# Kernel tuning notes

Hardware: AMD Instinct MI355X
Metric: run time of the kernel (lower is better)

Reference implementation:

```python
import jax, jax.numpy as jnp
import numpy as np

EMBED, HEADS, LEVELS, POINTS = 256, 8, 3, 4
HD = EMBED // HEADS
SHAPES = [(200, 200), (100, 100), (50, 50)]


def layer_norm(x, g, b, eps=1e-5):
    m = x.mean(-1, keepdims=True)
    v = ((x - m) ** 2).mean(-1, keepdims=True)
    return (x - m) * jax.lax.rsqrt(v + eps) * g + b


def bilinear_sample(v, loc, H, W):
    """v: (bs, H*W, heads, hd); loc: (bs, nq, heads, P, 2) normalized to [0,1].
    Matches F.grid_sample(bilinear, align_corners=False, padding_mode='zeros')
    applied to grid = 2*loc - 1. Returns (bs, nq, heads, P, hd)."""
    bs, nq, heads, P, _ = loc.shape
    hd = v.shape[-1]
    x = loc[..., 0] * W - 0.5
    y = loc[..., 1] * H - 0.5
    x0 = jnp.floor(x); y0 = jnp.floor(y)
    tx = x - x0; ty = y - y0
    x0i = x0.astype(jnp.int32); y0i = y0.astype(jnp.int32)
    vT = v.transpose(0, 2, 1, 3)  # (bs, heads, HW, hd)
    out = jnp.zeros((bs, heads, nq * P, hd), v.dtype)
    for dy, wy in ((0, 1.0 - ty), (1, ty)):
        for dx, wx in ((0, 1.0 - tx), (1, tx)):
            xi = x0i + dx; yi = y0i + dy
            valid = (xi >= 0) & (xi < W) & (yi >= 0) & (yi < H)
            idx = jnp.clip(yi, 0, H - 1) * W + jnp.clip(xi, 0, W - 1)
            w = (wx * wy * valid).transpose(0, 2, 1, 3).reshape(bs, heads, nq * P)
            idxT = idx.transpose(0, 2, 1, 3).reshape(bs, heads, nq * P)
            g = jnp.take_along_axis(vT, idxT[..., None], axis=2)  # (bs,heads,nqP,hd)
            out = out + w[..., None] * g
    return out.reshape(bs, heads, nq, P, hd).transpose(0, 2, 1, 3, 4)


def reference(query, value, query_pos, ref_pts, spatial_shapes, level_start_index,
              norm1_g, norm1_b, W_off, b_off, W_attn, b_attn, W_val, b_val,
              W_out, b_out, norm2_g, norm2_b, W1, b1, W2, b2):
    shapes = np.asarray(spatial_shapes)
    bs, nq, _ = query.shape
    # --- MultiScaleDeformableAttention on norm1(query) ---
    q = layer_norm(query, norm1_g, norm1_b)
    identity = q
    qp = q + query_pos
    offsets = (qp @ W_off + b_off).reshape(bs, nq, HEADS, LEVELS, POINTS, 2)
    aw = (qp @ W_attn + b_attn).reshape(bs, nq, HEADS, LEVELS * POINTS)
    aw = jax.nn.softmax(aw, axis=-1).reshape(bs, nq, HEADS, LEVELS, POINTS)
    v = (value @ W_val + b_val).reshape(bs, -1, HEADS, HD)
    # offset normalizer is (W, H) per level
    normalizer = jnp.stack([spatial_shapes[:, 1], spatial_shapes[:, 0]], -1).astype(query.dtype)
    loc = ref_pts[:, :, None, :, None, :] + offsets / normalizer[None, None, None, :, None, :]
    out = jnp.zeros((bs, nq, HEADS, HD), query.dtype)
    start = 0
    for l in range(LEVELS):
        H, W = int(shapes[l, 0]), int(shapes[l, 1])
        vl = v[:, start:start + H * W]
        s = bilinear_sample(vl, loc[:, :, :, l], H, W)  # (bs,nq,heads,P,hd)
        out = out + jnp.einsum('bqhpd,bqhp->bqhd', s, aw[:, :, :, l])
        start += H * W
    attn_out = out.reshape(bs, nq, EMBED) @ W_out + b_out + identity
    x = query + attn_out
    # --- FFN ---
    h = layer_norm(x, norm2_g, norm2_b)
    ffn = jax.nn.gelu(h @ W1 + b1, approximate=False) @ W2 + b2
    return x + ffn


def setup_inputs() -> dict:
    key = jax.random.key(0)
    ks = jax.random.split(key, 16)
    bs, nq = 1, 40000
    nv = sum(h * w for h, w in SHAPES)
    d = EMBED
    inp = {
        'query': jax.random.normal(ks[0], (bs, nq, d), jnp.float32),
        'value': jax.random.normal(ks[1], (bs, nv, d), jnp.float32),
        'query_pos': jax.random.normal(ks[2], (bs, nq, d), jnp.float32),
        'ref_pts': jax.random.uniform(ks[3], (bs, nq, LEVELS, 2), jnp.float32),
        'spatial_shapes': jnp.array(SHAPES, dtype=jnp.int32),
        'level_start_index': jnp.array(np.cumsum([0] + [h * w for h, w in SHAPES[:-1]]), dtype=jnp.int32),
    }
    s = 1.0 / np.sqrt(d)
    inp.update({
        'norm1_g': jnp.ones((d,), jnp.float32), 'norm1_b': jnp.zeros((d,), jnp.float32),
        'W_off': jax.random.normal(ks[4], (d, HEADS * LEVELS * POINTS * 2), jnp.float32) * 0.01,
        'b_off': jax.random.normal(ks[5], (HEADS * LEVELS * POINTS * 2,), jnp.float32) * 0.5,
        'W_attn': jax.random.normal(ks[6], (d, HEADS * LEVELS * POINTS), jnp.float32) * s,
        'b_attn': jnp.zeros((HEADS * LEVELS * POINTS,), jnp.float32),
        'W_val': jax.random.normal(ks[7], (d, d), jnp.float32) * s,
        'b_val': jnp.zeros((d,), jnp.float32),
        'W_out': jax.random.normal(ks[8], (d, d), jnp.float32) * s,
        'b_out': jnp.zeros((d,), jnp.float32),
        'norm2_g': jnp.ones((d,), jnp.float32), 'norm2_b': jnp.zeros((d,), jnp.float32),
        'W1': jax.random.normal(ks[9], (d, 4 * d), jnp.float32) * s,
        'b1': jnp.zeros((4 * d,), jnp.float32),
        'W2': jax.random.normal(ks[10], (4 * d, d), jnp.float32) / np.sqrt(4 * d),
        'b2': jnp.zeros((d,), jnp.float32),
    })
    return inp
```

## Files before the change

kernel.cpp:

```cpp
#include <hip/hip_runtime.h>
#include <hip/hip_bf16.h>
#include <math.h>

#define NQ 40000
#define NV 52500
#define D 256
#define NHEAD 8
#define HD 32
#define GUARD 512

using bf16x8 = __attribute__((ext_vector_type(8))) short;
using f32x4  = __attribute__((ext_vector_type(4))) float;
typedef int v2i32 __attribute__((ext_vector_type(2)));

__device__ __forceinline__ short f2bf(float f) {
  union { __hip_bfloat16 h; short s; } u;
  u.h = __float2bfloat16(f);
  return u.s;
}
__device__ __forceinline__ float bf2f(unsigned short s) {
  return __uint_as_float((unsigned)s << 16);
}
__device__ __forceinline__ unsigned pack2(float lo, float hi) {
  return (unsigned)(unsigned short)f2bf(lo) |
         ((unsigned)(unsigned short)f2bf(hi) << 16);
}
__device__ __forceinline__ void gload16(const void* g, void* l) {
  __builtin_amdgcn_global_load_lds(
      (const __attribute__((address_space(1))) unsigned int*)g,
      (__attribute__((address_space(3))) unsigned int*)l, 16, 0, 0);
}

template<int IMM>
__device__ __forceinline__ float swz_add(float x) {
  return x + __int_as_float(__builtin_amdgcn_ds_swizzle(__float_as_int(x), IMM));
}

__global__ __launch_bounds__(256) void k_prep(const float* __restrict__ Woff,
                                              const float* __restrict__ Wattn,
                                              const float* __restrict__ Wval,
                                              const float* __restrict__ Wout,
                                              const float* __restrict__ W1,
                                              const float* __restrict__ W2,
                                              const float* __restrict__ boff,
                                              const float* __restrict__ battn,
                                              short* __restrict__ WT288,
                                              short* __restrict__ WTval,
                                              short* __restrict__ WTout,
                                              short* __restrict__ WT1,
                                              short* __restrict__ WT2,
                                              float* __restrict__ bias288) {
  int idx = blockIdx.x * 256 + threadIdx.x;
  if (idx < 49152) {
    int n = idx >> 8, k = idx & 255;
    WT288[idx] = f2bf(Woff[k * 192 + n]);
  } else if (idx < 73728) {
    int li = idx - 49152; int n = li >> 8, k = li & 255;
    WT288[49152 + li] = f2bf(Wattn[k * 96 + n]);
  } else if (idx < 139264) {
    int li = idx - 73728; int n = li >> 8, k = li & 255;
    WTval[li] = f2bf(Wval[k * 256 + n]);
  } else if (idx < 204800) {
    int li = idx - 139264; int n = li >> 8, k = li & 255;
    WTout[li] = f2bf(Wout[k * 256 + n]);
  } else if (idx < 466944) {
    int li = idx - 204800; int n = li >> 8, k = li & 255;
    WT1[li] = f2bf(W1[k * 1024 + n]);
  } else if (idx < 729088) {
    int li = idx - 466944; int n = li >> 10, k = li & 1023;
    WT2[li] = f2bf(W2[k * 256 + n]);
  } else if (idx < 729376) {
    int i = idx - 729088;
    bias288[i] = (i < 192) ? boff[i] : battn[i - 192];
  }
}

__global__ __launch_bounds__(256) void k_ln1(const float* __restrict__ qin,
                                             const float* __restrict__ qpos,
                                             const float* __restrict__ g,
                                             const float* __restrict__ b,
                                             short* __restrict__ id_out,
                                             short* __restrict__ qp_out) {
  int wave = threadIdx.x >> 6;
  int lane = threadIdx.x & 63;
  int row  = blockIdx.x * 4 + wave;
  float4 x = ((const float4*)(qin + (size_t)row * D))[lane];
  float s  = x.x + x.y + x.z + x.w;
  float ss = x.x*x.x + x.y*x.y + x.z*x.z + x.w*x.w;
  for (int o = 32; o > 0; o >>= 1) { s += __shfl_down(s, o); ss += __shfl_down(ss, o); }
  s  = __shfl(s, 0);
  ss = __shfl(ss, 0);
  float m   = s * (1.0f / 256.0f);
  float var = ss * (1.0f / 256.0f) - m * m;
  float rs  = rsqrtf(var + 1e-5f);
  float4 gg = ((const float4*)g)[lane];
  float4 bb = ((const float4*)b)[lane];
  float4 qn;
  qn.x = (x.x - m) * rs * gg.x + bb.x;
  qn.y = (x.y - m) * rs * gg.y + bb.y;
  qn.z = (x.z - m) * rs * gg.z + bb.z;
  qn.w = (x.w - m) * rs * gg.w + bb.w;
  short4 io;
  io.x = f2bf(qn.x); io.y = f2bf(qn.y); io.z = f2bf(qn.z); io.w = f2bf(qn.w);
  ((short4*)(id_out + (size_t)row * D))[lane] = io;
  float4 p = ((const float4*)(qpos + (size_t)row * D))[lane];
  short4 o;
  o.x = f2bf(qn.x + p.x); o.y = f2bf(qn.y + p.y);
  o.z = f2bf(qn.z + p.z); o.w = f2bf(qn.w + p.w);
  ((short4*)(qp_out + (size_t)row * D))[lane] = o;
}

__global__ __launch_bounds__(256) void k_ln2(const float* __restrict__ xin,
                                             const float* __restrict__ g,
                                             const float* __restrict__ b,
                                             short* __restrict__ h_out) {
  int wave = threadIdx.x >> 6;
  int lane = threadIdx.x & 63;
  int row  = blockIdx.x * 4 + wave;
  float4 x = ((const float4*)(xin + (size_t)row * D))[lane];
  float s  = x.x + x.y + x.z + x.w;
  float ss = x.x*x.x + x.y*x.y + x.z*x.z + x.w*x.w;
  for (int o = 32; o > 0; o >>= 1) { s += __shfl_down(s, o); ss += __shfl_down(ss, o); }
  s  = __shfl(s, 0);
  ss = __shfl(ss, 0);
  float m   = s * (1.0f / 256.0f);
  float var = ss * (1.0f / 256.0f) - m * m;
  float rs  = rsqrtf(var + 1e-5f);
  float4 gg = ((const float4*)g)[lane];
  float4 bb = ((const float4*)b)[lane];
  short4 o;
  o.x = f2bf((x.x - m) * rs * gg.x + bb.x);
  o.y = f2bf((x.y - m) * rs * gg.y + bb.y);
  o.z = f2bf((x.z - m) * rs * gg.z + bb.z);
  o.w = f2bf((x.w - m) * rs * gg.w + bb.w);
  ((short4*)(h_out + (size_t)row * D))[lane] = o;
}

template<int EPI, int CVTA, int K>
__global__ __launch_bounds__(256) void k_gemm(const void* __restrict__ Ain,
                                              const short* __restrict__ WT,
                                              const float* __restrict__ bias,
                                              float* __restrict__ Cf,
                                              short* __restrict__ Cb,
                                              const float* __restrict__ R1,
                                              const float* __restrict__ R2,
                                              int M, int N) {
  constexpr int NT = K / 32;
  __shared__ short Al[3][4096];
  __shared__ short Bl[3][4096];
  const int tid = threadIdx.x;

  const int nbx = gridDim.x;
  const int nwg = nbx * gridDim.y;
  int flat = blockIdx.y * nbx + blockIdx.x;
  {
    int xcd = flat & 7, pos = flat >> 3;
    int qq = nwg >> 3, rr = nwg & 7;
    flat = (xcd < rr ? xcd * (qq + 1) : rr * (qq + 1) + (xcd - rr) * qq) + pos;
  }
  const int n0 = (flat % nbx) * 128, m0 = (flat / nbx) * 128;

  const int w = tid >> 6, l = tid & 63;
  const int wm = (w >> 1) * 64, wn = (w & 1) * 64;
  const int lr = l & 15;

  const int c0s = w * 2, c1s = c0s + 1;
  const int sr = l >> 2;
  const int sg = (((l & 3) ^ ((l >> 3) & 3)) << 3);
  const int ar0 = min(m0 + c0s * 16 + sr, M - 1);
  const int ar1 = min(m0 + c1s * 16 + sr, M - 1);
  const int br0 = min(n0 + c0s * 16 + sr, N - 1);
  const int br1 = min(n0 + c1s * 16 + sr, N - 1);
  const short* bP0 = WT + (size_t)br0 * K + sg;
  const short* bP1 = WT + (size_t)br1 * K + sg;
  const short* aP0 = (const short*)Ain + (size_t)ar0 * K + sg;
  const short* aP1 = (const short*)Ain + (size_t)ar1 * K + sg;
  const float* aF0 = (const float*)Ain + (size_t)ar0 * K + sg;
  const float* aF1 = (const float*)Ain + (size_t)ar1 * K + sg;
  short* wD0 = &Al[0][(c0s * 16 + sr) * 32 + ((l & 3) << 3)];
  short* wD1 = &Al[0][(c1s * 16 + sr) * 32 + ((l & 3) << 3)];

  const int fsw = (((l >> 4) ^ ((l >> 1) & 3)) << 3);
  const int aRd = (wm + lr) * 32 + fsw;
  const int bRd = (wn + lr) * 32 + fsw;

  f32x4 acc[4][4];
#pragma unroll
  for (int i = 0; i < 4; ++i)
#pragma unroll
    for (int j = 0; j < 4; ++j) acc[i][j] = (f32x4){0, 0, 0, 0};

  if (CVTA) {
    {
      float4 f00 = *(const float4*)(aF0);
      float4 f01 = *(const float4*)(aF0 + 4);
      float4 f10 = *(const float4*)(aF1);
      float4 f11 = *(const float4*)(aF1 + 4);
      int4 p0, p1;
      p0.x = pack2(f00.x, f00.y); p0.y = pack2(f00.z, f00.w);
      p0.z = pack2(f01.x, f01.y); p0.w = pack2(f01.z, f01.w);
      p1.x = pack2(f10.x, f10.y); p1.y = pack2(f10.z, f10.w);
      p1.z = pack2(f11.x, f11.y); p1.w = pack2(f11.z, f11.w);
      *(int4*)wD0 = p0;
      *(int4*)wD1 = p1;
      gload16(bP0, &Bl[0][c0s * 512]);
      gload16(bP1, &Bl[0][c1s * 512]);
      __syncthreads();
    }
#pragma unroll 2
    for (int t = 0; t < NT - 1; ++t) {
      const int buf = t & 1, nbuf = buf ^ 1;
      const int kn = (t + 1) * 32;
      float4 f00 = *(const float4*)(aF0 + kn);
      float4 f01 = *(const float4*)(aF0 + kn + 4);
      float4 f10 = *(const float4*)(aF1 + kn);
      float4 f11 = *(const float4*)(aF1 + kn + 4);
      gload16(bP0 + kn, &Bl[nbuf][c0s * 512]);
      gload16(bP1 + kn, &Bl[nbuf][c1s * 512]);

      bf16x8 af[4], bfr[4];
#pragma unroll
      for (int i = 0; i < 4; ++i) {
        af[i]  = *(const bf16x8*)&Al[buf][aRd + i * 512];
        bfr[i] = *(const bf16x8*)&Bl[buf][bRd + i * 512];
      }
#pragma unroll
      for (int i = 0; i < 4; ++i)
#pragma unroll
        for (int j = 0; j < 4; ++j)
          acc[i][j] = __builtin_amdgcn_mfma_f32_16x16x32_bf16(af[i], bfr[j], acc[i][j], 0, 0, 0);

      int4 p0, p1;
      p0.x = pack2(f00.x, f00.y); p0.y = pack2(f00.z, f00.w);
      p0.z = pack2(f01.x, f01.y); p0.w = pack2(f01.z, f01.w);
      p1.x = pack2(f10.x, f10.y); p1.y = pack2(f10.z, f10.w);
      p1.z = pack2(f11.x, f11.y); p1.w = pack2(f11.z, f11.w);
      *(int4*)(wD0 + nbuf * 4096) = p0;
      *(int4*)(wD1 + nbuf * 4096) = p1;
      __syncthreads();
    }
    {
      const int buf = (NT - 1) & 1;
      bf16x8 af[4], bfr[4];
#pragma unroll
      for (int i = 0; i < 4; ++i) {
        af[i]  = *(const bf16x8*)&Al[buf][aRd + i * 512];
        bfr[i] = *(const bf16x8*)&Bl[buf][bRd + i * 512];
      }
#pragma unroll
      for (int i = 0; i < 4; ++i)
#pragma unroll
        for (int j = 0; j < 4; ++j)
          acc[i][j] = __builtin_amdgcn_mfma_f32_16x16x32_bf16(af[i], bfr[j], acc[i][j], 0, 0, 0);
    }
  } else {
    gload16(aP0, &Al[0][c0s * 512]);
    gload16(aP1, &Al[0][c1s * 512]);
    gload16(bP0, &Bl[0][c0s * 512]);
    gload16(bP1, &Bl[0][c1s * 512]);
    if (NT > 1) {
      gload16(aP0 + 32, &Al[1][c0s * 512]);
      gload16(aP1 + 32, &Al[1][c1s * 512]);
      gload16(bP0 + 32, &Bl[1][c0s * 512]);
      gload16(bP1 + 32, &Bl[1][c1s * 512]);
    }
#pragma unroll
    for (int t = 0; t < NT; ++t) {
      const int buf = t % 3;
      if (t + 1 < NT) asm volatile("s_waitcnt vmcnt(4)" ::: "memory");
      else            asm volatile("s_waitcnt vmcnt(0)" ::: "memory");
      __builtin_amdgcn_s_barrier();
      __builtin_amdgcn_sched_barrier(0);
      if (t + 2 < NT) {
        const int kn = (t + 2) * 32, nb = (t + 2) % 3;
        gload16(aP0 + kn, &Al[nb][c0s * 512]);
        gload16(aP1 + kn, &Al[nb][c1s * 512]);
        gload16(bP0 + kn, &Bl[nb][c0s * 512]);
        gload16(bP1 + kn, &Bl[nb][c1s * 512]);
      }
      bf16x8 af[4], bfr[4];
#pragma unroll
      for (int i = 0; i < 4; ++i) {
        af[i]  = *(const bf16x8*)&Al[buf][aRd + i * 512];
        bfr[i] = *(const bf16x8*)&Bl[buf][bRd + i * 512];
      }
      __builtin_amdgcn_s_setprio(1);
#pragma unroll
      for (int i = 0; i < 4; ++i)
#pragma unroll
        for (int j = 0; j < 4; ++j)
          acc[i][j] = __builtin_amdgcn_mfma_f32_16x16x32_bf16(af[i], bfr[j], acc[i][j], 0, 0, 0);
      __builtin_amdgcn_s_setprio(0);
    }
  }

  __syncthreads();
  float* wsc = (float*)&Al[0][0] + w * 1088;
  const unsigned short* R2b = (const unsigned short*)R2;
  const int rr2 = l >> 2;
  const int cp4 = (l & 3) << 2;
  float bsv[16];
#pragma unroll
  for (int p = 0; p < 4; ++p) {
    int col = n0 + wn + p * 16 + cp4;
    float4 bv = {0, 0, 0, 0};
    if (col < N) bv = *(const float4*)&bias[col];
    bsv[p*4+0] = bv.x; bsv[p*4+1] = bv.y; bsv[p*4+2] = bv.z; bsv[p*4+3] = bv.w;
  }
  const int ec2 = l & 15, er2 = (l >> 4) << 2;
#pragma unroll
  for (int i = 0; i < 4; ++i) {
#pragma unroll
    for (int j = 0; j < 4; ++j)
#pragma unroll
      for (int r = 0; r < 4; ++r)
        wsc[(er2 + r) * 68 + j * 16 + ec2] = acc[i][j][r];
    const int grow = m0 + wm + i * 16 + rr2;
    if (grow < M) {
#pragma unroll
      for (int p = 0; p < 4; ++p) {
        int col = n0 + wn + p * 16 + cp4;
        if (col >= N) continue;
        float4 vv = *(const float4*)&wsc[rr2 * 68 + p * 16 + cp4];
        float v0 = vv.x + bsv[p*4+0];
        float v1 = vv.y + bsv[p*4+1];
        float v2 = vv.z + bsv[p*4+2];
        float v3 = vv.w + bsv[p*4+3];
        size_t base = (size_t)grow * N + col;
        if (EPI == 0) {
          *(float4*)&Cf[base] = (float4){v0, v1, v2, v3};
        } else if (EPI == 1) {
          float u0 = v0 * (2.3021178f + 0.1029445f * v0 * v0);
          float u1 = v1 * (2.3021178f + 0.1029445f * v1 * v1);
          float u2 = v2 * (2.3021178f + 0.1029445f * v2 * v2);
          float u3 = v3 * (2.3021178f + 0.1029445f * v3 * v3);
          float g0 = v0 - v0 / (1.0f + exp2f(u0));
          float g1 = v1 - v1 / (1.0f + exp2f(u1));
          float g2 = v2 - v2 / (1.0f + exp2f(u2));
          float g3 = v3 - v3 / (1.0f + exp2f(u3));
          *(uint2*)&Cb[base] = (uint2){pack2(g0, g1), pack2(g2, g3)};
        } else if (EPI == 5) {
          float4 r1 = *(const float4*)&R1[base];
          uint2 rb = *(const uint2*)&R2b[base];
          *(float4*)&Cf[base] = (float4){
              v0 + r1.x + __uint_as_float(rb.x << 16),
              v1 + r1.y + __uint_as_float(rb.x & 0xffff0000u),
              v2 + r1.z + __uint_as_float(rb.y << 16),
              v3 + r1.w + __uint_as_float(rb.y & 0xffff0000u)};
        } else if (EPI == 3) {
          float4 cur = *(const float4*)&Cf[base];
          *(float4*)&Cf[base] =
              (float4){cur.x + v0, cur.y + v1, cur.z + v2, cur.w + v3};
        } else {
          *(uint2*)&Cb[base] = (uint2){pack2(v0, v1), pack2(v2, v3)};
        }
      }
    }
  }
}

__global__ __launch_bounds__(256) void k_post(const unsigned short* __restrict__ res,
                                              const float* __restrict__ refp,
                                              int* __restrict__ idxB,
                                              unsigned short* __restrict__ wT) {
  int t = blockIdx.x * 256 + threadIdx.x;
  if (t >= NQ * 8) return;
  int q = t >> 3, h = t & 7;
  const unsigned short* rr = res + (size_t)q * 288;
  const unsigned short* lg = rr + 192 + h * 12;
  float lf[12];
#pragma unroll
  for (int i = 0; i < 12; ++i) lf[i] = bf2f(lg[i]);
  float mx = lf[0];
#pragma unroll
  for (int i = 1; i < 12; ++i) mx = fmaxf(mx, lf[i]);
  float e[12]; float sum = 0.0f;
#pragma unroll
  for (int i = 0; i < 12; ++i) { e[i] = expf(lf[i] - mx); sum += e[i]; }
  float inv = 1.0f / sum;

  const float dims[3] = {200.0f, 100.0f, 50.0f};
  const int   sts[3]  = {0, 40000, 50000};
  int* idq = idxB + (size_t)t * 16;
  unsigned short* wq = wT + (size_t)t * 64;
#pragma unroll
  for (int l = 0; l < 3; ++l) {
    const int W = (int)dims[l];
    const float fW = dims[l];
    float rx = refp[((size_t)q * 3 + l) * 2 + 0];
    float ry = refp[((size_t)q * 3 + l) * 2 + 1];
    float invd = 1.0f / fW;
#pragma unroll
    for (int p = 0; p < 4; ++p) {
      int j = ((h * 3 + l) * 4 + p) * 2;
      float lx = rx + bf2f(rr[j + 0]) * invd;
      float ly = ry + bf2f(rr[j + 1]) * invd;
      float fx = lx * fW - 0.5f;
      float fy = ly * fW - 0.5f;
      float x0f = floorf(fx), y0f = floorf(fy);
      float tx = fx - x0f, ty = fy - y0f;
      int x0 = (int)x0f, y0 = (int)y0f;
      bool vx0 = (unsigned)x0       < (unsigned)W;
      bool vx1 = (unsigned)(x0 + 1) < (unsigned)W;
      bool vy0 = (unsigned)y0       < (unsigned)W;
      bool vy1 = (unsigned)(y0 + 1) < (unsigned)W;
      float a = e[l * 4 + p] * inv;
      float w00 = (vx0 && vy0) ? a * (1.0f - tx) * (1.0f - ty) : 0.0f;
      float w01 = (vx1 && vy0) ? a * tx * (1.0f - ty) : 0.0f;
      float w10 = (vx0 && vy1) ? a * (1.0f - tx) * ty : 0.0f;
      float w11 = (vx1 && vy1) ? a * tx * ty : 0.0f;
      int pt = l * 4 + p;
      idq[pt] = sts[l] + y0 * W + x0;
      wq[0 * 16 + pt] = (unsigned short)f2bf(w00);
      wq[1 * 16 + pt] = (unsigned short)f2bf(w01);
      wq[2 * 16 + pt] = (unsigned short)f2bf(w10);
      wq[3 * 16 + pt] = (unsigned short)f2bf(w11);
    }
  }
}

__global__ __launch_bounds__(256) void k_sample(const short* __restrict__ vprojG,
                                                const int* __restrict__ idxB,
                                                const unsigned short* __restrict__ wT,
                                                short* __restrict__ smp) {
  const int lane = threadIdx.x & 63;
  const int slot = lane >> 4;
  const int qh   = blockIdx.x * 16 + (threadIdx.x >> 6) * 4 + slot;
  const int tap  = (lane >> 2) & 3;
  const int cq   = lane & 3;
  const int h = qh & 7;
  const int dy = tap >> 1, dx = tap & 1;
  const short* vb = vprojG + (size_t)GUARD * D + h * HD + cq * 8;

  const int myidx = idxB[(size_t)qh * 16 + (lane & 15)];
  const unsigned short* wp = wT + ((size_t)qh * 4 + tap) * 16;
  uint4 w8 = *(const uint4*)wp;
  uint2 w4 = *(const uint2*)(wp + 8);
  const unsigned wd[6] = {w8.x, w8.y, w8.z, w8.w, w4.x, w4.y};

  float acc[8];
#pragma unroll
  for (int j = 0; j < 8; ++j) acc[j] = 0.0f;

  const int Dim[3] = {200, 100, 50};
  const int slotbase = slot << 4;
#pragma unroll
  for (int it = 0; it < 12; ++it) {
    const int W = Dim[it >> 2];
    int idx0 = __builtin_amdgcn_ds_bpermute((slotbase + it) << 2, myidx);
    int idx = idx0 + dy * W + dx;
    unsigned wraw = wd[it >> 1];
    float wgt = __uint_as_float((it & 1) ? (wraw & 0xffff0000u) : (wraw << 16));
    uint4 v = *(const uint4*)(vb + (ptrdiff_t)idx * D);
    acc[0] = fmaf(wgt, __uint_as_float(v.x << 16),         acc[0]);
    acc[1] = fmaf(wgt, __uint_as_float(v.x & 0xffff0000u), acc[1]);
    acc[2] = fmaf(wgt, __uint_as_float(v.y << 16),         acc[2]);
    acc[3] = fmaf(wgt, __uint_as_float(v.y & 0xffff0000u), acc[3]);
    acc[4] = fmaf(wgt, __uint_as_float(v.z << 16),         acc[4]);
    acc[5] = fmaf(wgt, __uint_as_float(v.z & 0xffff0000u), acc[5]);
    acc[6] = fmaf(wgt, __uint_as_float(v.w << 16),         acc[6]);
    acc[7] = fmaf(wgt, __uint_as_float(v.w & 0xffff0000u), acc[7]);
  }

#pragma unroll
  for (int j = 0; j < 8; ++j) {
    float a = swz_add<0x101F>(acc[j]);
    acc[j] = swz_add<0x201F>(a);
  }

  if (tap == 0) {
    uint4 o;
    o.x = pack2(acc[0], acc[1]);
    o.y = pack2(acc[2], acc[3]);
    o.z = pack2(acc[4], acc[5]);
    o.w = pack2(acc[6], acc[7]);
    *(uint4*)(smp + (size_t)qh * HD + cq * 8) = o;
  }
}

extern "C" void kernel_launch(void* const* d_in, const int* in_sizes, int n_in,
                              void* d_out, int out_size, void* d_ws, size_t ws_size,
                              hipStream_t stream) {
  const float* query  = (const float*)d_in[0];
  const float* value  = (const float*)d_in[1];
  const float* qpos   = (const float*)d_in[2];
  const float* refp   = (const float*)d_in[3];
  const float* n1g = (const float*)d_in[6];
  const float* n1b = (const float*)d_in[7];
  const float* Woff = (const float*)d_in[8];
  const float* boff = (const float*)d_in[9];
  const float* Wattn = (const float*)d_in[10];
  const float* battn = (const float*)d_in[11];
  const float* Wval = (const float*)d_in[12];
  const float* bval = (const float*)d_in[13];
  const float* Wout = (const float*)d_in[14];
  const float* bout = (const float*)d_in[15];
  const float* n2g = (const float*)d_in[16];
  const float* n2b = (const float*)d_in[17];
  const float* W1 = (const float*)d_in[18];
  const float* b1 = (const float*)d_in[19];
  const float* W2 = (const float*)d_in[20];
  const float* b2 = (const float*)d_in[21];

  float* out = (float*)d_out;
  char* Wb = (char*)d_ws;

  short* qp_bf   = (short*)Wb;
  short* iden_bf = (short*)(Wb + 20480000);
  int*   idxB    = (int*)(Wb + 40960000);
  unsigned short* wT = (unsigned short*)(Wb + 61440000);
  short* res_bf  = (short*)(Wb + 102400000);
  short* vprjG   = (short*)(Wb + 102400000);
  short* vprj_bf = (short*)(Wb + 102400000 + GUARD * D * 2);
  short* h_bf    = (short*)(Wb + 102400000);
  short* smp_bf  = (short*)(Wb + 130000000);
  short* mid_bf  = (short*)Wb;
  char*  Wbase   = Wb + 150600000;
  short* WT288   = (short*)(Wbase);
  short* WTval   = (short*)(Wbase + 147456);
  short* WTout   = (short*)(Wbase + 278528);
  short* WT1     = (short*)(Wbase + 409600);
  short* WT2     = (short*)(Wbase + 933888);
  float* bias288 = (float*)(Wbase + 1458176);

  k_prep<<<(729376 + 255) / 256, 256, 0, stream>>>(
      Woff, Wattn, Wval, Wout, W1, W2, boff, battn,
      WT288, WTval, WTout, WT1, WT2, bias288);

  k_ln1<<<NQ / 4, 256, 0, stream>>>(query, qpos, n1g, n1b, iden_bf, qp_bf);

  k_gemm<4,0,256><<<dim3(3, (NQ + 127) / 128), 256, 0, stream>>>(
      qp_bf, WT288, bias288, nullptr, res_bf, nullptr, nullptr, NQ, 288);
  k_post<<<(NQ * 8 + 255) / 256, 256, 0, stream>>>(
      (const unsigned short*)res_bf, refp, idxB, wT);

  k_gemm<4,1,256><<<dim3(2, (NV + 127) / 128), 256, 0, stream>>>(
      value, WTval, bval, nullptr, vprj_bf, nullptr, nullptr, NV, 256);

  k_sample<<<NQ * NHEAD / 16, 256, 0, stream>>>(vprjG, idxB, wT, smp_bf);

  k_gemm<5,0,256><<<dim3(2, (NQ + 127) / 128), 256, 0, stream>>>(
      smp_bf, WTout, bout, out, nullptr, query, (const float*)iden_bf, NQ, 256);

  k_ln2<<<NQ / 4, 256, 0, stream>>>(out, n2g, n2b, h_bf);

  k_gemm<1,0,256><<<dim3(8, (NQ + 127) / 128), 256, 0, stream>>>(
      h_bf, WT1, b1, nullptr, mid_bf, nullptr, nullptr, NQ, 1024);

  k_gemm<3,0,1024><<<dim3(2, (NQ + 127) / 128), 256, 0, stream>>>(
      mid_bf, WT2, b2, out, nullptr, nullptr, nullptr, NQ, 256);
}
```

Before: 335.2 us.

## Fuse FFN GEMMs into one kernel keeping GELU intermediate in LDS

Replaces the two FFN GEMM launches (up-projection with GELU, then down-projection with residual add) with a single kernel. Each 128-row tile computes 128-column chunks of the hidden activation, applies GELU into shared memory, and immediately accumulates them into the down-projection. This removes the bf16 round-trip of the 40000x1024 intermediate through global memory and one launch. The trade-off is a large register footprint (32 accumulator vectors plus 16), heavy LDS use limiting occupancy to one block per CU, and only 313 blocks. The generic GEMM epilogue scratch stride also changes from 68 to 76 floats, likely to reduce LDS bank conflicts.

```diff
diff --git a/kernel.cpp b/kernel.cpp
--- a/kernel.cpp
+++ b/kernel.cpp
@@ -295,7 +295,7 @@
   }
 
   __syncthreads();
-  float* wsc = (float*)&Al[0][0] + w * 1088;
+  float* wsc = (float*)&Al[0][0] + w * 1216;
   const unsigned short* R2b = (const unsigned short*)R2;
   const int rr2 = l >> 2;
   const int cp4 = (l & 3) << 2;
@@ -314,14 +314,14 @@
     for (int j = 0; j < 4; ++j)
 #pragma unroll
       for (int r = 0; r < 4; ++r)
-        wsc[(er2 + r) * 68 + j * 16 + ec2] = acc[i][j][r];
+        wsc[(er2 + r) * 76 + j * 16 + ec2] = acc[i][j][r];
     const int grow = m0 + wm + i * 16 + rr2;
     if (grow < M) {
 #pragma unroll
       for (int p = 0; p < 4; ++p) {
         int col = n0 + wn + p * 16 + cp4;
         if (col >= N) continue;
-        float4 vv = *(const float4*)&wsc[rr2 * 68 + p * 16 + cp4];
+        float4 vv = *(const float4*)&wsc[rr2 * 76 + p * 16 + cp4];
         float v0 = vv.x + bsv[p*4+0];
         float v1 = vv.y + bsv[p*4+1];
         float v2 = vv.z + bsv[p*4+2];
@@ -359,6 +359,182 @@
   }
 }
 
+__global__ __launch_bounds__(256, 1) void k_ffn(const short* __restrict__ h,
+                                                const short* __restrict__ WT1,
+                                                const float* __restrict__ b1,
+                                                const short* __restrict__ WT2,
+                                                const float* __restrict__ b2,
+                                                float* __restrict__ x, int M) {
+  __shared__ short hA[3][4096];
+  __shared__ short W1S[3][4096];
+  __shared__ short W2S[3][8192];
+  __shared__ short midT[16384];
+  const int tid = threadIdx.x;
+
+  int flat = blockIdx.x;
+  {
+    int nwg = gridDim.x;
+    int xcd = flat & 7, pos = flat >> 3;
+    int qq = nwg >> 3, rr = nwg & 7;
+    flat = (xcd < rr ? xcd * (qq + 1) : rr * (qq + 1) + (xcd - rr) * qq) + pos;
+  }
+  const int m0 = flat * 128;
+
+  const int w = tid >> 6, l = tid & 63;
+  const int lr = l & 15, ec = l & 15;
+  const int c0s = w * 2, c1s = c0s + 1;
+  const int sr = l >> 2;
+  const int sg = (((l & 3) ^ ((l >> 3) & 3)) << 3);
+  const int ar0 = min(m0 + c0s * 16 + sr, M - 1);
+  const int ar1 = min(m0 + c1s * 16 + sr, M - 1);
+  const short* aP0 = h + (size_t)ar0 * 256 + sg;
+  const short* aP1 = h + (size_t)ar1 * 256 + sg;
+  const int fsw = (((l >> 4) ^ ((l >> 1) & 3)) << 3);
+  const int a1Rd = (w * 32 + lr) * 32 + fsw;
+  const int bRd  = lr * 32 + fsw;
+  short* midW = &midT[w * 4096];
+  const int w2row = w * 64 + (l >> 2);
+  const int erq = (l >> 4) << 2;
+
+  f32x4 acc2[2][16];
+#pragma unroll
+  for (int i = 0; i < 2; ++i)
+#pragma unroll
+    for (int j = 0; j < 16; ++j) acc2[i][j] = (f32x4){0, 0, 0, 0};
+
+  for (int c = 0; c < 8; ++c) {
+    const short* w1P0 = WT1 + (size_t)(c * 128 + c0s * 16 + sr) * 256 + sg;
+    const short* w1P1 = WT1 + (size_t)(c * 128 + c1s * 16 + sr) * 256 + sg;
+    gload16(aP0,       &hA[0][c0s * 512]);
+    gload16(aP1,       &hA[0][c1s * 512]);
+    gload16(w1P0,      &W1S[0][c0s * 512]);
+    gload16(w1P1,      &W1S[0][c1s * 512]);
+    gload16(aP0 + 32,  &hA[1][c0s * 512]);
+    gload16(aP1 + 32,  &hA[1][c1s * 512]);
+    gload16(w1P0 + 32, &W1S[1][c0s * 512]);
+    gload16(w1P1 + 32, &W1S[1][c1s * 512]);
+
+    f32x4 acc1[2][8];
+#pragma unroll
+    for (int i = 0; i < 2; ++i)
+#pragma unroll
+      for (int j = 0; j < 8; ++j) acc1[i][j] = (f32x4){0, 0, 0, 0};
+
+#pragma unroll
+    for (int t = 0; t < 8; ++t) {
+      if (t < 7) asm volatile("s_waitcnt vmcnt(4)" ::: "memory");
+      else       asm volatile("s_waitcnt vmcnt(0)" ::: "memory");
+      __builtin_amdgcn_s_barrier();
+      __builtin_amdgcn_sched_barrier(0);
+      if (t + 2 < 8) {
+        const int kn = (t + 2) * 32, nb = (t + 2) % 3;
+        gload16(aP0 + kn,  &hA[nb][c0s * 512]);
+        gload16(aP1 + kn,  &hA[nb][c1s * 512]);
+        gload16(w1P0 + kn, &W1S[nb][c0s * 512]);
+        gload16(w1P1 + kn, &W1S[nb][c1s * 512]);
+      }
+      const int buf = t % 3;
+      bf16x8 af[2], bf[8];
+      af[0] = *(const bf16x8*)&hA[buf][a1Rd];
+      af[1] = *(const bf16x8*)&hA[buf][a1Rd + 512];
+#pragma unroll
+      for (int j = 0; j < 8; ++j) bf[j] = *(const bf16x8*)&W1S[buf][bRd + j * 512];
+      __builtin_amdgcn_s_setprio(1);
+#pragma unroll
+      for (int i = 0; i < 2; ++i)
+#pragma unroll
+        for (int j = 0; j < 8; ++j)
+          acc1[i][j] = __builtin_amdgcn_mfma_f32_16x16x32_bf16(af[i], bf[j], acc1[i][j], 0, 0, 0);
+      __builtin_amdgcn_s_setprio(0);
+    }
+
+#pragma unroll
+    for (int q = 0; q < 4; ++q)
+      gload16(WT2 + (size_t)(w2row + q * 16) * 1024 + c * 128 + 0 + sg,
+              &W2S[0][(w * 64 + q * 16) * 32 + (l & 3) * 8]);
+#pragma unroll
+    for (int q = 0; q < 4; ++q)
+      gload16(WT2 + (size_t)(w2row + q * 16) * 1024 + c * 128 + 32 + sg,
+              &W2S[1][(w * 64 + q * 16) * 32 + (l & 3) * 8]);
+
+    {
+      float b1v[8];
+#pragma unroll
+      for (int j = 0; j < 8; ++j) b1v[j] = b1[c * 128 + j * 16 + ec];
+#pragma unroll
+      for (int i = 0; i < 2; ++i)
+#pragma unroll
+        for (int j = 0; j < 8; ++j) {
+          const int t2 = j >> 1;
+#pragma unroll
+          for (int r = 0; r < 4; ++r) {
+            float v = acc1[i][j][r] + b1v[j];
+            float u = v * (2.3021178f + 0.1029445f * v * v);
+            float g = v - v / (1.0f + exp2f(u));
+            int rowl = i * 16 + erq + r;
+            int s = ((j & 1) * 2 + (ec >> 3)) ^ ((rowl >> 1) & 3);
+            midW[t2 * 1024 + rowl * 32 + s * 8 + (l & 7)] = f2bf(g);
+          }
+        }
+    }
+
+#pragma unroll
+    for (int t2 = 0; t2 < 4; ++t2) {
+      if (t2 < 3) asm volatile("s_waitcnt vmcnt(4)" ::: "memory");
+      else        asm volatile("s_waitcnt vmcnt(0)" ::: "memory");
+      __builtin_amdgcn_s_barrier();
+      __builtin_amdgcn_sched_barrier(0);
+      if (t2 + 2 < 4) {
+        const int nb = (t2 + 2) % 3, kn = c * 128 + (t2 + 2) * 32;
+#pragma unroll
+        for (int q = 0; q < 4; ++q)
+          gload16(WT2 + (size_t)(w2row + q * 16) * 1024 + kn + sg,
+                  &W2S[nb][(w * 64 + q * 16) * 32 + (l & 3) * 8]);
+      }
+      const int buf = t2 % 3;
+      bf16x8 af[2], bf[16];
+      af[0] = *(const bf16x8*)&midW[t2 * 1024 + lr * 32 + fsw];
+      af[1] = *(const bf16x8*)&midW[t2 * 1024 + (16 + lr) * 32 + fsw];
+#pragma unroll
+      for (int j = 0; j < 16; ++j) bf[j] = *(const bf16x8*)&W2S[buf][bRd + j * 512];
+      __builtin_amdgcn_s_setprio(1);
+#pragma unroll
+      for (int i = 0; i < 2; ++i)
+#pragma unroll
+        for (int j = 0; j < 16; ++j)
+          acc2[i][j] = __builtin_amdgcn_mfma_f32_16x16x32_bf16(af[i], bf[j], acc2[i][j], 0, 0, 0);
+      __builtin_amdgcn_s_setprio(0);
+    }
+  }
+
+  float* scr = (float*)midW;
+  const int row16 = l >> 2;
+#pragma unroll
+  for (int i = 0; i < 2; ++i) {
+#pragma unroll
+    for (int jq = 0; jq < 4; ++jq) {
+#pragma unroll
+      for (int jj = 0; jj < 4; ++jj)
+#pragma unroll
+        for (int r = 0; r < 4; ++r)
+          scr[(erq + r) * 68 + jj * 16 + ec] = acc2[i][jq * 4 + jj][r];
+      const int grow = m0 + w * 32 + i * 16 + row16;
+      if (grow < M) {
+#pragma unroll
+        for (int c4 = 0; c4 < 4; ++c4) {
+          const int gcol = jq * 64 + (l & 3) * 16 + c4 * 4;
+          float4 vv = *(const float4*)&scr[row16 * 68 + (l & 3) * 16 + c4 * 4];
+          float4 bb = *(const float4*)&b2[gcol];
+          size_t base = (size_t)grow * 256 + gcol;
+          float4 cur = *(const float4*)&x[base];
+          *(float4*)&x[base] = (float4){cur.x + vv.x + bb.x, cur.y + vv.y + bb.y,
+                                        cur.z + vv.z + bb.z, cur.w + vv.w + bb.w};
+        }
+      }
+    }
+  }
+}
+
 __global__ __launch_bounds__(256) void k_post(const unsigned short* __restrict__ res,
                                               const float* __restrict__ refp,
                                               int* __restrict__ idxB,
@@ -514,7 +690,6 @@
   short* vprj_bf = (short*)(Wb + 102400000 + GUARD * D * 2);
   short* h_bf    = (short*)(Wb + 102400000);
   short* smp_bf  = (short*)(Wb + 130000000);
-  short* mid_bf  = (short*)Wb;
   char*  Wbase   = Wb + 150600000;
   short* WT288   = (short*)(Wbase);
   short* WTval   = (short*)(Wbase + 147456);
@@ -544,9 +719,5 @@
 
   k_ln2<<<NQ / 4, 256, 0, stream>>>(out, n2g, n2b, h_bf);
 
-  k_gemm<1,0,256><<<dim3(8, (NQ + 127) / 128), 256, 0, stream>>>(
-      h_bf, WT1, b1, nullptr, mid_bf, nullptr, nullptr, NQ, 1024);
-
-  k_gemm<3,0,1024><<<dim3(2, (NQ + 127) / 128), 256, 0, stream>>>(
-      mid_bf, WT2, b2, out, nullptr, nullptr, nullptr, NQ, 256);
-}
+  k_ffn<<<(NQ + 127) / 128, 256, 0, stream>>>(h_bf, WT1, b1, WT2, b2, out, NQ);
+}
```

New measurement: 438.4 us. +30.8%, slower.
